# Kernel optimization log

Hardware: AMD Instinct MI355X
Metric: run time of the kernel (lower is better)

The kernel has to match this reference:

```python
import jax, jax.numpy as jnp
import numpy as np

N_NODES = 50000
N_EDGES = 800000
NFEAT = 512
NHID = 64
NHEADS = 8
NCLASS = 40
ALPHA = 0.2  # LeakyReLU slope
EPS = 1e-16  # guards isolated-node division


def setup_inputs() -> dict:
    key = jax.random.key(0)
    k = jax.random.split(key, 6)
    x = jax.random.normal(k[0], (N_NODES, NFEAT), dtype=jnp.float32)
    W_heads = jax.random.normal(k[1], (NHEADS, NFEAT, NHID), dtype=jnp.float32) * 0.05
    a_heads = jax.random.normal(k[2], (NHEADS, 2 * NHID), dtype=jnp.float32) * 0.05
    W_out = jax.random.normal(k[3], (NHEADS * NHID, NCLASS), dtype=jnp.float32) * 0.05
    a_out = jax.random.normal(k[4], (2 * NCLASS,), dtype=jnp.float32) * 0.05
    edge_index = jax.random.randint(k[5], (2, N_EDGES), 0, N_NODES, dtype=jnp.int32)
    return {"x": x, "W_heads": W_heads, "a_heads": a_heads,
            "W_out": W_out, "a_out": a_out, "edge_index": edge_index}


def _gat_layer(x, W, a, row, col, concat):
    # pyGAT sparse layer: h = xW; e_ij = exp(-LeakyReLU(a^T [h_i || h_j]));
    # out_i = sum_j e_ij h_j / sum_j e_ij   (aggregate into row, gather from col)
    D = W.shape[1]
    h = x @ W                                            # [N, D]
    score = h[row] @ a[:D] + h[col] @ a[D:]              # [E]
    e = jnp.exp(-jax.nn.leaky_relu(score, ALPHA))        # [E]
    num = jax.ops.segment_sum(e[:, None] * h[col], row, num_segments=x.shape[0])  # [N, D]
    den = jax.ops.segment_sum(e, row, num_segments=x.shape[0])                    # [N]
    out = num / (den[:, None] + EPS)
    return jax.nn.elu(out) if concat else out


def reference(x, W_heads, a_heads, W_out, a_out, edge_index):
    # dropout layers are identity in eval mode (training=False)
    row, col = edge_index[0], edge_index[1]
    heads = jax.vmap(lambda W, a: _gat_layer(x, W, a, row, col, True))(W_heads, a_heads)
    # [H, N, D] -> [N, H*D] (concat along feature dim, head-major like torch.cat)
    hcat = jnp.transpose(heads, (1, 0, 2)).reshape(x.shape[0], -1)
    return _gat_layer(hcat, W_out, a_out, row, col, False)  # [N, NCLASS]
```

## Files before the change

kernel.cpp:

```cpp
#include <hip/hip_runtime.h>
#include <hip/hip_bf16.h>

#define N_NODES 50000
#define N_EDGES 800000
#define NFEAT   512
#define NHID    64
#define NHEADS  8
#define NCLASS  40
#define HD      (NHEADS*NHID)
#define ALPHA   0.2f
#define EPS_F   1e-16f
#define NCHUNK  ((N_NODES + 255)/256)

typedef __attribute__((ext_vector_type(8))) short short8;
typedef __attribute__((ext_vector_type(4))) float floatx4;

__device__ __forceinline__ float bf2f(unsigned short u) {
    union { unsigned int i; float f; } v; v.i = ((unsigned int)u) << 16; return v.f;
}
__device__ __forceinline__ unsigned short f2bf(float f) {
    union { __hip_bfloat16 h; unsigned short u; } cv;
    cv.h = __float2bfloat16(f);
    return cv.u;
}

__global__ void repackWb(const float* __restrict__ Wh, unsigned short* __restrict__ Wrb,
                         int* __restrict__ deg) {
    int idx = blockIdx.x*256 + threadIdx.x;
    if (idx < N_NODES) deg[idx] = 0;
    if (idx >= 512*512) return;
    int n = idx >> 9, k = idx & 511;
    int hd = n >> 6, d = n & 63;
    Wrb[idx] = f2bf(Wh[(size_t)hd*NFEAT*NHID + (size_t)k*NHID + d]);
}

__global__ void repackWout(const float* __restrict__ Wo, unsigned short* __restrict__ Wob) {
    int idx = blockIdx.x*256 + threadIdx.x;
    if (idx >= 64*512) return;
    int n = idx >> 9, k = idx & 511;
    float v = (n < NCLASS) ? Wo[(size_t)k*NCLASS + n] : 0.f;
    Wob[idx] = f2bf(v);
}

__global__ __launch_bounds__(512, 2) void mfma_gemm1(const float* __restrict__ A,
                                                     const unsigned short* __restrict__ Bbf,
                                                     unsigned short* __restrict__ H1p, int M) {
    __shared__ short Asl[128*40];
    __shared__ short Bsl[512*40];
    int tid  = threadIdx.x;
    int wid  = tid >> 6, lane = tid & 63;
    int lrow = lane & 15, quad = lane >> 4;
    int wm = wid & 1, wn = wid >> 1;
    int row0 = blockIdx.x * 128;
    if (row0 >= M) return;

    floatx4 acc[4][8];
#pragma unroll
    for (int mm = 0; mm < 4; mm++)
#pragma unroll
        for (int nn = 0; nn < 8; nn++) acc[mm][nn] = (floatx4){0.f,0.f,0.f,0.f};

    for (int k0 = 0; k0 < 512; k0 += 32) {
        {
            int r = tid >> 2, kk = (tid & 3) * 8;
            int ar = row0 + r; ar = ar < M ? ar : M - 1;
            const float* src = A + (size_t)ar*512 + k0 + kk;
            float4 f0 = *(const float4*)src;
            float4 f1 = *(const float4*)(src + 4);
            short8 h;
            h[0] = (short)f2bf(f0.x); h[1] = (short)f2bf(f0.y);
            h[2] = (short)f2bf(f0.z); h[3] = (short)f2bf(f0.w);
            h[4] = (short)f2bf(f1.x); h[5] = (short)f2bf(f1.y);
            h[6] = (short)f2bf(f1.z); h[7] = (short)f2bf(f1.w);
            *(short8*)(&Asl[r*40 + kk]) = h;
        }
#pragma unroll
        for (int it = 0; it < 4; ++it) {
            int q = tid + it*512;
            int r = q >> 2, kk = (q & 3) * 8;
            *(short8*)(&Bsl[r*40 + kk]) =
                *(const short8*)(Bbf + (size_t)r*512 + k0 + kk);
        }
        __syncthreads();
        short8 af[4], bfr[8];
#pragma unroll
        for (int mm = 0; mm < 4; ++mm)
            af[mm] = *(const short8*)(&Asl[(wm*64 + mm*16 + lrow)*40 + quad*8]);
#pragma unroll
        for (int nn = 0; nn < 8; ++nn)
            bfr[nn] = *(const short8*)(&Bsl[(wn*128 + nn*16 + lrow)*40 + quad*8]);
#pragma unroll
        for (int mm = 0; mm < 4; ++mm)
#pragma unroll
            for (int nn = 0; nn < 8; ++nn)
                acc[mm][nn] = __builtin_amdgcn_mfma_f32_16x16x32_bf16(
                    af[mm], bfr[nn], acc[mm][nn], 0, 0, 0);
        __syncthreads();
    }

#pragma unroll
    for (int mm = 0; mm < 4; ++mm) {
        int rbase = row0 + wm*64 + mm*16 + quad*4;
#pragma unroll
        for (int nn = 0; nn < 8; ++nn) {
            int c = wn*128 + nn*16 + lrow;
            int off = (c & 63)*8 + (c >> 6);
#pragma unroll
            for (int r = 0; r < 4; ++r) {
                int grow = rbase + r;
                if (grow < M)
                    H1p[(size_t)grow*512 + off] = f2bf(acc[mm][nn][r]);
            }
        }
    }
}

__global__ __launch_bounds__(256) void mfma_gemm2(const unsigned short* __restrict__ Abf,
                                                  const unsigned short* __restrict__ Bbf,
                                                  float* __restrict__ H2p, int M) {
    __shared__ short Asl[256*40];
    __shared__ short Bsl[64*40];
    int tid  = threadIdx.x;
    int wid  = tid >> 6, lane = tid & 63;
    int lrow = lane & 15, quad = lane >> 4;
    int row0 = blockIdx.x * 256;

    floatx4 acc[4][4];
#pragma unroll
    for (int mm = 0; mm < 4; mm++)
#pragma unroll
        for (int nn = 0; nn < 4; nn++) acc[mm][nn] = (floatx4){0.f,0.f,0.f,0.f};

    for (int k0 = 0; k0 < 512; k0 += 32) {
#pragma unroll
        for (int it = 0; it < 4; ++it) {
            int q  = tid + it*256;
            int r  = q >> 2, kk = (q & 3) * 8;
            int ar = row0 + r; ar = ar < M ? ar : M - 1;
            *(short8*)(&Asl[r*40 + kk]) =
                *(const short8*)(Abf + (size_t)ar*512 + k0 + kk);
        }
        {
            int r = tid >> 2, kk = (tid & 3) * 8;
            *(short8*)(&Bsl[r*40 + kk]) =
                *(const short8*)(Bbf + (size_t)r*512 + k0 + kk);
        }
        __syncthreads();
        short8 af[4], bfr[4];
#pragma unroll
        for (int mm = 0; mm < 4; ++mm)
            af[mm] = *(const short8*)(&Asl[(wid*64 + mm*16 + lrow)*40 + quad*8]);
#pragma unroll
        for (int nn = 0; nn < 4; ++nn)
            bfr[nn] = *(const short8*)(&Bsl[(nn*16 + lrow)*40 + quad*8]);
#pragma unroll
        for (int mm = 0; mm < 4; ++mm)
#pragma unroll
            for (int nn = 0; nn < 4; ++nn)
                acc[mm][nn] = __builtin_amdgcn_mfma_f32_16x16x32_bf16(
                    af[mm], bfr[nn], acc[mm][nn], 0, 0, 0);
        __syncthreads();
    }

#pragma unroll
    for (int mm = 0; mm < 4; ++mm) {
        int rbase = row0 + wid*64 + mm*16 + quad*4;
#pragma unroll
        for (int nn = 0; nn < 4; ++nn) {
            int c = nn*16 + lrow;
#pragma unroll
            for (int r = 0; r < 4; ++r) {
                int grow = rbase + r;
                if (grow < M)
                    H2p[(size_t)grow*64 + c] = acc[mm][nn][r];
            }
        }
    }
}

__global__ __launch_bounds__(256) void dots1(const unsigned short* __restrict__ H1p,
                                             const float* __restrict__ a_heads,
                                             float* __restrict__ srcdot,
                                             float* __restrict__ dstdot) {
    int wave = (blockIdx.x*256 + threadIdx.x) >> 6;
    int lane = threadIdx.x & 63;
    if (wave >= N_NODES) return;
    short8 hv = *(const short8*)(H1p + (size_t)wave*512 + lane*8);
    float s0[8], s1[8];
#pragma unroll
    for (int j = 0; j < 8; j++) {
        float h = bf2f((unsigned short)hv[j]);
        s0[j] = h * a_heads[j*128 + lane];
        s1[j] = h * a_heads[j*128 + 64 + lane];
    }
#pragma unroll
    for (int off = 32; off > 0; off >>= 1) {
#pragma unroll
        for (int j = 0; j < 8; j++) {
            s0[j] += __shfl_down(s0[j], off, 64);
            s1[j] += __shfl_down(s1[j], off, 64);
        }
    }
    if (lane == 0) {
#pragma unroll
        for (int j = 0; j < 8; j++) {
            srcdot[wave*8 + j] = s0[j];
            dstdot[wave*8 + j] = s1[j];
        }
    }
}

__global__ void histk(const int* __restrict__ row, int* __restrict__ deg) {
    int e = blockIdx.x*256 + threadIdx.x;
    if (e < N_EDGES) atomicAdd(&deg[row[e]], 1);
}
__global__ void scanA(const int* __restrict__ deg, int* __restrict__ row_ptr,
                      int* __restrict__ chunk_tot) {
    __shared__ int s[256];
    int t = threadIdx.x;
    int idx = blockIdx.x*256 + t;
    int v = (idx < N_NODES) ? deg[idx] : 0;
    s[t] = v;
    __syncthreads();
#pragma unroll
    for (int off = 1; off < 256; off <<= 1) {
        int x = (t >= off) ? s[t-off] : 0;
        __syncthreads();
        s[t] += x;
        __syncthreads();
    }
    if (idx < N_NODES) row_ptr[idx] = s[t] - v;
    if (t == 255) chunk_tot[blockIdx.x] = s[t];
}
__global__ void scanB(const int* __restrict__ chunk_tot, int* __restrict__ chunk_off,
                      int* __restrict__ row_ptr) {
    __shared__ int s[256];
    int t = threadIdx.x;
    int v = (t < NCHUNK) ? chunk_tot[t] : 0;
    s[t] = v;
    __syncthreads();
#pragma unroll
    for (int off = 1; off < 256; off <<= 1) {
        int x = (t >= off) ? s[t-off] : 0;
        __syncthreads();
        s[t] += x;
        __syncthreads();
    }
    if (t < NCHUNK) chunk_off[t] = s[t] - v;
    if (t == 255) row_ptr[N_NODES] = s[t];
}
__global__ void scanC(const int* __restrict__ chunk_off, int* __restrict__ row_ptr,
                      int* __restrict__ cursor) {
    int idx = blockIdx.x*256 + threadIdx.x;
    if (idx < N_NODES) {
        int rp = row_ptr[idx] + chunk_off[idx >> 8];
        row_ptr[idx] = rp;
        cursor[idx] = rp;
    }
}

__global__ void fillk_w1(const int* __restrict__ row, const int* __restrict__ col,
                         const float* __restrict__ srcdot, const float* __restrict__ dstdot,
                         int* __restrict__ cursor, int* __restrict__ csr_col,
                         float* __restrict__ Wcsr) {
    int e = blockIdx.x*256 + threadIdx.x;
    if (e >= N_EDGES) return;
    int r = row[e], c = col[e];
    int pos = atomicAdd(&cursor[r], 1);
    csr_col[pos] = c;
    float4 sa = *(const float4*)(srcdot + (size_t)r*8);
    float4 sb = *(const float4*)(srcdot + (size_t)r*8 + 4);
    float4 da = *(const float4*)(dstdot + (size_t)c*8);
    float4 db = *(const float4*)(dstdot + (size_t)c*8 + 4);
    float s[8] = {sa.x+da.x, sa.y+da.y, sa.z+da.z, sa.w+da.w,
                  sb.x+db.x, sb.y+db.y, sb.z+db.z, sb.w+db.w};
    float o[8];
#pragma unroll
    for (int j = 0; j < 8; j++) {
        float lr = s[j] > 0.f ? s[j] : ALPHA*s[j];
        o[j] = __expf(-lr);
    }
    *(float4*)(Wcsr + (size_t)pos*8)     = make_float4(o[0], o[1], o[2], o[3]);
    *(float4*)(Wcsr + (size_t)pos*8 + 4) = make_float4(o[4], o[5], o[6], o[7]);
}

__global__ __launch_bounds__(256) void agg1(const unsigned short* __restrict__ H1p,
                                            const float* __restrict__ Wcsr,
                                            const int* __restrict__ row_ptr,
                                            const int* __restrict__ csr_col,
                                            unsigned short* __restrict__ hcatb) {
    int wave = (blockIdx.x*256 + threadIdx.x) >> 6;
    int lane = threadIdx.x & 63;
    if (wave >= N_NODES) return;
    int start = row_ptr[wave], end = row_ptr[wave+1];
    float acc[8], den[8];
#pragma unroll
    for (int j = 0; j < 8; j++) { acc[j] = 0.f; den[j] = 0.f; }

    int k = start;
    for (; k + 4 <= end; k += 4) {
        int c0 = csr_col[k],   c1 = csr_col[k+1];
        int c2 = csr_col[k+2], c3 = csr_col[k+3];
        short8 hv0 = *(const short8*)(H1p + (size_t)c0*512 + lane*8);
        short8 hv1 = *(const short8*)(H1p + (size_t)c1*512 + lane*8);
        short8 hv2 = *(const short8*)(H1p + (size_t)c2*512 + lane*8);
        short8 hv3 = *(const short8*)(H1p + (size_t)c3*512 + lane*8);
        float4 wv[8];
#pragma unroll
        for (int q = 0; q < 8; q++)
            wv[q] = *(const float4*)(Wcsr + (size_t)k*8 + q*4);
        const float* w0 = (const float*)&wv[0];
        const float* w1 = (const float*)&wv[2];
        const float* w2 = (const float*)&wv[4];
        const float* w3 = (const float*)&wv[6];
#pragma unroll
        for (int j = 0; j < 8; j++) {
            den[j] += (w0[j] + w1[j]) + (w2[j] + w3[j]);
            acc[j] = fmaf(w0[j], bf2f((unsigned short)hv0[j]), acc[j]);
            acc[j] = fmaf(w1[j], bf2f((unsigned short)hv1[j]), acc[j]);
            acc[j] = fmaf(w2[j], bf2f((unsigned short)hv2[j]), acc[j]);
            acc[j] = fmaf(w3[j], bf2f((unsigned short)hv3[j]), acc[j]);
        }
    }
    for (; k < end; ++k) {
        int c = csr_col[k];
        float4 wa = *(const float4*)(Wcsr + (size_t)k*8);
        float4 wb = *(const float4*)(Wcsr + (size_t)k*8 + 4);
        short8 hv = *(const short8*)(H1p + (size_t)c*512 + lane*8);
        float w[8] = {wa.x, wa.y, wa.z, wa.w, wb.x, wb.y, wb.z, wb.w};
#pragma unroll
        for (int j = 0; j < 8; j++) {
            den[j] += w[j];
            acc[j] = fmaf(w[j], bf2f((unsigned short)hv[j]), acc[j]);
        }
    }
#pragma unroll
    for (int j = 0; j < 8; j++) {
        float o = acc[j] / (den[j] + EPS_F);
        o = o > 0.f ? o : (__expf(o) - 1.f);
        hcatb[(size_t)wave*HD + j*64 + lane] = f2bf(o);
    }
}

__global__ void dots2(const float* __restrict__ H2p, const float* __restrict__ a_out,
                      float* __restrict__ src2, float* __restrict__ dst2) {
    int i = blockIdx.x*256 + threadIdx.x;
    if (i >= N_NODES) return;
    float s0 = 0.f, s1 = 0.f;
#pragma unroll
    for (int c = 0; c < NCLASS; c++) {
        float h = H2p[(size_t)i*64 + c];
        s0 = fmaf(h, a_out[c], s0);
        s1 = fmaf(h, a_out[NCLASS + c], s1);
    }
    src2[i] = s0; dst2[i] = s1;
}

__global__ __launch_bounds__(256) void agg2(const float* __restrict__ H2p,
                                            const float* __restrict__ src2,
                                            const float* __restrict__ dst2,
                                            const int* __restrict__ row_ptr,
                                            const int* __restrict__ csr_col,
                                            float* __restrict__ out) {
    int wave = (blockIdx.x*256 + threadIdx.x) >> 6;
    int lane = threadIdx.x & 63;
    if (wave >= N_NODES) return;
    int start = row_ptr[wave], end = row_ptr[wave+1];
    float s2i = src2[wave];
    int l = lane < NCLASS ? lane : 0;
    float acc = 0.f, den = 0.f;
    int k = start;
    for (; k + 4 <= end; k += 4) {
        int c0 = csr_col[k],   c1 = csr_col[k+1];
        int c2 = csr_col[k+2], c3 = csr_col[k+3];
        float t0 = s2i + dst2[c0], t1 = s2i + dst2[c1];
        float t2 = s2i + dst2[c2], t3 = s2i + dst2[c3];
        float h0 = H2p[(size_t)c0*64 + l];
        float h1 = H2p[(size_t)c1*64 + l];
        float h2 = H2p[(size_t)c2*64 + l];
        float h3 = H2p[(size_t)c3*64 + l];
        t0 = t0 > 0.f ? t0 : ALPHA*t0;  float w0 = __expf(-t0);
        t1 = t1 > 0.f ? t1 : ALPHA*t1;  float w1 = __expf(-t1);
        t2 = t2 > 0.f ? t2 : ALPHA*t2;  float w2 = __expf(-t2);
        t3 = t3 > 0.f ? t3 : ALPHA*t3;  float w3 = __expf(-t3);
        den += (w0 + w1) + (w2 + w3);
        acc = fmaf(w0, h0, acc);
        acc = fmaf(w1, h1, acc);
        acc = fmaf(w2, h2, acc);
        acc = fmaf(w3, h3, acc);
    }
    for (; k < end; ++k) {
        int c = csr_col[k];
        float t = s2i + dst2[c];
        t = t > 0.f ? t : ALPHA*t;
        float w = __expf(-t);
        den += w;
        acc = fmaf(w, H2p[(size_t)c*64 + l], acc);
    }
    if (lane < NCLASS)
        out[(size_t)wave*NCLASS + lane] = acc / (den + EPS_F);
}

extern "C" void kernel_launch(void* const* d_in, const int* in_sizes, int n_in,
                              void* d_out, int out_size, void* d_ws, size_t ws_size,
                              hipStream_t stream) {
    const float* x       = (const float*)d_in[0];
    const float* W_heads = (const float*)d_in[1];
    const float* a_heads = (const float*)d_in[2];
    const float* W_out   = (const float*)d_in[3];
    const float* a_out   = (const float*)d_in[4];
    const int*   ei      = (const int*)d_in[5];
    const int*   row     = ei;
    const int*   col     = ei + N_EDGES;
    float* out = (float*)d_out;

    char* ws = (char*)d_ws;
    size_t off = 0;
    auto alloc = [&](size_t bytes) {
        char* p = ws + off;
        off = (off + bytes + 255) & ~(size_t)255;
        return p;
    };
    unsigned short* Wrb   = (unsigned short*)alloc((size_t)512*512*2);
    unsigned short* Wob   = (unsigned short*)alloc((size_t)64*512*2);
    unsigned short* H1p   = (unsigned short*)alloc((size_t)N_NODES*HD*2);
    unsigned short* hcatb = (unsigned short*)alloc((size_t)N_NODES*HD*2);
    float* srcdot  = (float*)alloc((size_t)N_NODES*NHEADS*4);
    float* dstdot  = (float*)alloc((size_t)N_NODES*NHEADS*4);
    float* Wcsr    = (float*)alloc((size_t)N_EDGES*NHEADS*4);
    int*   deg     = (int*)alloc((size_t)N_NODES*4);
    int*   row_ptr = (int*)alloc((size_t)(N_NODES+1)*4);
    int*   cursor  = (int*)alloc((size_t)N_NODES*4);
    int*   ctot    = (int*)alloc(256*4);
    int*   coff    = (int*)alloc(256*4);
    int*   csr_col = (int*)alloc((size_t)N_EDGES*4);
    float* H2p     = (float*)alloc((size_t)N_NODES*64*4);
    float* src2    = (float*)alloc((size_t)N_NODES*4);
    float* dst2    = (float*)alloc((size_t)N_NODES*4);
    (void)ws_size;

    const int EB = (N_EDGES + 255)/256;
    const int WB = (N_NODES*64 + 255)/256;
    const int NB = (N_NODES + 255)/256;

    repackWb<<<(512*512 + 255)/256, 256, 0, stream>>>(W_heads, Wrb, deg);
    repackWout<<<(64*512 + 255)/256, 256, 0, stream>>>(W_out, Wob);
    mfma_gemm1<<<(N_NODES + 127)/128, 512, 0, stream>>>(x, Wrb, H1p, N_NODES);
    dots1<<<WB, 256, 0, stream>>>(H1p, a_heads, srcdot, dstdot);

    histk<<<EB, 256, 0, stream>>>(row, deg);
    scanA<<<NCHUNK, 256, 0, stream>>>(deg, row_ptr, ctot);
    scanB<<<1, 256, 0, stream>>>(ctot, coff, row_ptr);
    scanC<<<NCHUNK, 256, 0, stream>>>(coff, row_ptr, cursor);
    fillk_w1<<<EB, 256, 0, stream>>>(row, col, srcdot, dstdot, cursor,
                                     csr_col, Wcsr);

    agg1<<<WB, 256, 0, stream>>>(H1p, Wcsr, row_ptr, csr_col, hcatb);

    mfma_gemm2<<<(N_NODES + 255)/256, 256, 0, stream>>>(hcatb, Wob, H2p, N_NODES);
    dots2<<<NB, 256, 0, stream>>>(H2p, a_out, src2, dst2);
    agg2<<<WB, 256, 0, stream>>>(H2p, src2, dst2, row_ptr, csr_col, out);
}
```

Measured before the change: 561.7 us.

## Retile first GEMM into 128x128 tiles with grouped order and register prefetch

The first projection GEMM moves from one 512-thread block covering all 512 output columns per 128-row tile to 256-thread blocks covering 128x128 tiles. Block IDs are grouped so that 8 row tiles share each column tile, which should help A rows stay in L2 across the four column blocks. Global loads for the next k-slice are prefetched into registers while the MFMAs for the current slice run, so load latency overlaps compute. Each block now does less work and needs fewer accumulators, which allows more occupancy, but x is read and converted to bf16 four times instead of once. The two weight-repack kernels are also merged into one launch.

```diff
diff --git a/kernel.cpp b/kernel.cpp
--- a/kernel.cpp
+++ b/kernel.cpp
@@ -24,75 +24,102 @@
     return cv.u;
 }
 
-__global__ void repackWb(const float* __restrict__ Wh, unsigned short* __restrict__ Wrb,
-                         int* __restrict__ deg) {
+__global__ void prep(const float* __restrict__ Wh, unsigned short* __restrict__ Wrb,
+                     const float* __restrict__ Wo, unsigned short* __restrict__ Wob,
+                     int* __restrict__ deg) {
     int idx = blockIdx.x*256 + threadIdx.x;
+    if (idx >= 512*512) return;
     if (idx < N_NODES) deg[idx] = 0;
-    if (idx >= 512*512) return;
-    int n = idx >> 9, k = idx & 511;
-    int hd = n >> 6, d = n & 63;
-    Wrb[idx] = f2bf(Wh[(size_t)hd*NFEAT*NHID + (size_t)k*NHID + d]);
-}
-
-__global__ void repackWout(const float* __restrict__ Wo, unsigned short* __restrict__ Wob) {
-    int idx = blockIdx.x*256 + threadIdx.x;
-    if (idx >= 64*512) return;
-    int n = idx >> 9, k = idx & 511;
-    float v = (n < NCLASS) ? Wo[(size_t)k*NCLASS + n] : 0.f;
-    Wob[idx] = f2bf(v);
-}
-
-__global__ __launch_bounds__(512, 2) void mfma_gemm1(const float* __restrict__ A,
-                                                     const unsigned short* __restrict__ Bbf,
-                                                     unsigned short* __restrict__ H1p, int M) {
+    {
+        int n = idx >> 9, k = idx & 511;
+        int hd = n >> 6, d = n & 63;
+        Wrb[idx] = f2bf(Wh[(size_t)hd*NFEAT*NHID + (size_t)k*NHID + d]);
+    }
+    if (idx < 64*512) {
+        int n = idx >> 9, k = idx & 511;
+        float v = (n < NCLASS) ? Wo[(size_t)k*NCLASS + n] : 0.f;
+        Wob[idx] = f2bf(v);
+    }
+}
+
+__global__ __launch_bounds__(256) void mfma_gemm1(const float* __restrict__ A,
+                                                  const unsigned short* __restrict__ Bbf,
+                                                  unsigned short* __restrict__ H1p, int M) {
+    int id = blockIdx.x;
+    int rb = (id >> 5)*8 + (id & 7);
+    int cb = (id >> 3) & 3;
+    int row0 = rb * 128, col0 = cb * 128;
+    if (row0 >= M) return;
+
     __shared__ short Asl[128*40];
-    __shared__ short Bsl[512*40];
+    __shared__ short Bsl[128*40];
     int tid  = threadIdx.x;
     int wid  = tid >> 6, lane = tid & 63;
     int lrow = lane & 15, quad = lane >> 4;
     int wm = wid & 1, wn = wid >> 1;
-    int row0 = blockIdx.x * 128;
-    if (row0 >= M) return;
-
-    floatx4 acc[4][8];
+
+    int sr[2], sk[2];
+#pragma unroll
+    for (int it = 0; it < 2; ++it) {
+        int q = tid + it*256;
+        sr[it] = q >> 2; sk[it] = (q & 3) * 8;
+    }
+    int arow[2];
+#pragma unroll
+    for (int it = 0; it < 2; ++it) {
+        int ar = row0 + sr[it];
+        arow[it] = ar < M ? ar : M - 1;
+    }
+
+    floatx4 acc[4][4];
 #pragma unroll
     for (int mm = 0; mm < 4; mm++)
 #pragma unroll
-        for (int nn = 0; nn < 8; nn++) acc[mm][nn] = (floatx4){0.f,0.f,0.f,0.f};
+        for (int nn = 0; nn < 4; nn++) acc[mm][nn] = (floatx4){0.f,0.f,0.f,0.f};
+
+    float4 fa[2][2];
+    short8 fb[2];
+#pragma unroll
+    for (int it = 0; it < 2; ++it) {
+        const float* src = A + (size_t)arow[it]*512 + sk[it];
+        fa[it][0] = *(const float4*)src;
+        fa[it][1] = *(const float4*)(src + 4);
+        fb[it] = *(const short8*)(Bbf + (size_t)(col0 + sr[it])*512 + sk[it]);
+    }
 
     for (int k0 = 0; k0 < 512; k0 += 32) {
-        {
-            int r = tid >> 2, kk = (tid & 3) * 8;
-            int ar = row0 + r; ar = ar < M ? ar : M - 1;
-            const float* src = A + (size_t)ar*512 + k0 + kk;
-            float4 f0 = *(const float4*)src;
-            float4 f1 = *(const float4*)(src + 4);
+#pragma unroll
+        for (int it = 0; it < 2; ++it) {
             short8 h;
-            h[0] = (short)f2bf(f0.x); h[1] = (short)f2bf(f0.y);
-            h[2] = (short)f2bf(f0.z); h[3] = (short)f2bf(f0.w);
-            h[4] = (short)f2bf(f1.x); h[5] = (short)f2bf(f1.y);
-            h[6] = (short)f2bf(f1.z); h[7] = (short)f2bf(f1.w);
-            *(short8*)(&Asl[r*40 + kk]) = h;
-        }
-#pragma unroll
-        for (int it = 0; it < 4; ++it) {
-            int q = tid + it*512;
-            int r = q >> 2, kk = (q & 3) * 8;
-            *(short8*)(&Bsl[r*40 + kk]) =
-                *(const short8*)(Bbf + (size_t)r*512 + k0 + kk);
-        }
-        __syncthreads();
-        short8 af[4], bfr[8];
+            h[0] = (short)f2bf(fa[it][0].x); h[1] = (short)f2bf(fa[it][0].y);
+            h[2] = (short)f2bf(fa[it][0].z); h[3] = (short)f2bf(fa[it][0].w);
+            h[4] = (short)f2bf(fa[it][1].x); h[5] = (short)f2bf(fa[it][1].y);
+            h[6] = (short)f2bf(fa[it][1].z); h[7] = (short)f2bf(fa[it][1].w);
+            *(short8*)(&Asl[sr[it]*40 + sk[it]]) = h;
+            *(short8*)(&Bsl[sr[it]*40 + sk[it]]) = fb[it];
+        }
+        __syncthreads();
+        if (k0 + 32 < 512) {
+            int kn = k0 + 32;
+#pragma unroll
+            for (int it = 0; it < 2; ++it) {
+                const float* src = A + (size_t)arow[it]*512 + kn + sk[it];
+                fa[it][0] = *(const float4*)src;
+                fa[it][1] = *(const float4*)(src + 4);
+                fb[it] = *(const short8*)(Bbf + (size_t)(col0 + sr[it])*512 + kn + sk[it]);
+            }
+        }
+        short8 af[4], bfr[4];
 #pragma unroll
         for (int mm = 0; mm < 4; ++mm)
             af[mm] = *(const short8*)(&Asl[(wm*64 + mm*16 + lrow)*40 + quad*8]);
 #pragma unroll
-        for (int nn = 0; nn < 8; ++nn)
-            bfr[nn] = *(const short8*)(&Bsl[(wn*128 + nn*16 + lrow)*40 + quad*8]);
+        for (int nn = 0; nn < 4; ++nn)
+            bfr[nn] = *(const short8*)(&Bsl[(wn*64 + nn*16 + lrow)*40 + quad*8]);
 #pragma unroll
         for (int mm = 0; mm < 4; ++mm)
 #pragma unroll
-            for (int nn = 0; nn < 8; ++nn)
+            for (int nn = 0; nn < 4; ++nn)
                 acc[mm][nn] = __builtin_amdgcn_mfma_f32_16x16x32_bf16(
                     af[mm], bfr[nn], acc[mm][nn], 0, 0, 0);
         __syncthreads();
@@ -102,8 +129,8 @@
     for (int mm = 0; mm < 4; ++mm) {
         int rbase = row0 + wm*64 + mm*16 + quad*4;
 #pragma unroll
-        for (int nn = 0; nn < 8; ++nn) {
-            int c = wn*128 + nn*16 + lrow;
+        for (int nn = 0; nn < 4; ++nn) {
+            int c = col0 + wn*64 + nn*16 + lrow;
             int off = (c & 63)*8 + (c >> 6);
 #pragma unroll
             for (int r = 0; r < 4; ++r) {
@@ -443,9 +470,12 @@
     const int WB = (N_NODES*64 + 255)/256;
     const int NB = (N_NODES + 255)/256;
 
-    repackWb<<<(512*512 + 255)/256, 256, 0, stream>>>(W_heads, Wrb, deg);
-    repackWout<<<(64*512 + 255)/256, 256, 0, stream>>>(W_out, Wob);
-    mfma_gemm1<<<(N_NODES + 127)/128, 512, 0, stream>>>(x, Wrb, H1p, N_NODES);
+    prep<<<(512*512 + 255)/256, 256, 0, stream>>>(W_heads, Wrb, W_out, Wob, deg);
+    {
+        int rtiles = (N_NODES + 127)/128;
+        int nblk = ((rtiles + 7)/8) * 32;
+        mfma_gemm1<<<nblk, 256, 0, stream>>>(x, Wrb, H1p, N_NODES);
+    }
     dots1<<<WB, 256, 0, stream>>>(H1p, a_heads, srcdot, dstdot);
 
     histk<<<EB, 256, 0, stream>>>(row, deg);
```

Measured after the change: 553.8 us. About the same (-1.4%).
